# Kernel optimization log

Measured on AMD Instinct MI355X. Metric: run time of the kernel, lower is better.

Reference implementation:

```python
import jax, jax.numpy as jnp
import numpy as np
import math

N_HEADS = 12
HEAD_SIZE = 64
D_MODEL = 768
N_BASIS = 256
LENGTH = 1024
BATCH = 8
INV_SQRT_2PI = 1.0 / math.sqrt(2.0 * math.pi)


def _phi(t):
    # standard normal pdf
    return INV_SQRT_2PI * jnp.exp(-0.5 * t * t)


def _make_basis():
    # get_gaussian_basis_functions: meshgrid(linspace(0,1,N/2), sigmas).flatten()
    sigmas = np.array([0.01, 0.05], dtype=np.float32)
    mus = np.linspace(0.0, 1.0, N_BASIS // 2, dtype=np.float32)
    mu_b = np.repeat(mus, 2)          # [N]
    sigma_b = np.tile(sigmas, N_BASIS // 2)  # [N]
    return jnp.asarray(mu_b), jnp.asarray(sigma_b)


def _make_G(mu_b, sigma_b, klen, ridge=1.0):
    # compute_G: positions (i+1)/l, F[j,i] = psi_j(pos_i), G = F^T (F F^T + I)^{-1}
    pos = jnp.arange(1, klen + 1, dtype=jnp.float32) / klen
    F = _phi((pos[None, :] - mu_b[:, None]) / sigma_b[:, None]) / sigma_b[:, None]  # [N, klen]
    A = F @ F.T + ridge * jnp.eye(N_BASIS, dtype=jnp.float32)
    return F.T @ jnp.linalg.inv(A)  # [klen, N]


def setup_inputs() -> dict:
    key = jax.random.key(0)
    ks = jax.random.split(key, 8)
    sc = 1.0 / math.sqrt(D_MODEL)
    x = jax.random.normal(ks[0], (LENGTH, BATCH, D_MODEL), jnp.float32)
    q = jax.random.normal(ks[1], (LENGTH, BATCH, D_MODEL), jnp.float32)
    Wq = jax.random.normal(ks[2], (D_MODEL, D_MODEL), jnp.float32) * sc
    Wk = jax.random.normal(ks[3], (D_MODEL, D_MODEL), jnp.float32) * sc
    Wv = jax.random.normal(ks[4], (D_MODEL, D_MODEL), jnp.float32) * sc
    Wo = jax.random.normal(ks[5], (D_MODEL, D_MODEL), jnp.float32) * sc
    w_mu = jax.random.normal(ks[6], (N_BASIS,), jnp.float32) * (1.0 / math.sqrt(N_BASIS))
    w_sigma = jax.random.normal(ks[7], (N_BASIS,), jnp.float32) * (1.0 / math.sqrt(N_BASIS))
    mu_b, sigma_b = _make_basis()
    G = _make_G(mu_b, sigma_b, LENGTH)
    return {"x": x, "q": q, "Wq": Wq, "Wk": Wk, "Wv": Wv, "Wo": Wo,
            "w_mu": w_mu, "w_sigma": w_sigma, "mu_b": mu_b, "sigma_b": sigma_b, "G": G}


def reference(x, q, Wq, Wk, Wv, Wo, w_mu, w_sigma, mu_b, sigma_b, G):
    klen, B, d = x.shape
    qlen = q.shape[0]
    H, dh = N_HEADS, HEAD_SIZE
    # value_function: compress memory onto basis coefficients, B_mat: [B, N, d]
    Bmat = jnp.einsum('lbd,ln->bnd', x, G)
    keys = (Bmat @ Wk.T).reshape(B, N_BASIS, H, dh).transpose(0, 2, 1, 3)    # [B,H,N,dh]
    values = (Bmat @ Wv.T).reshape(B, N_BASIS, H, dh).transpose(0, 2, 1, 3)  # [B,H,N,dh]
    query = (q.transpose(1, 0, 2) @ Wq.T).reshape(B, qlen, H, dh).transpose(0, 2, 1, 3)
    scores = jnp.einsum('bhqe,bhne->bhqn', query, keys) / math.sqrt(dh)      # [B,H,q,N]
    # attention distribution parameters (theta -> (mu, sigma_sq) exactly)
    mu = jax.nn.sigmoid(scores @ w_mu)          # [B,H,q]
    sigma_sq = jax.nn.softplus(scores @ w_sigma)  # [B,H,q]
    # ContinuousSoftmax forward: E_{N(mu,sigma_sq)}[psi_j]
    #   = N(mu; mu_b_j, sigma_b_j^2 + sigma_sq)   (product-of-Gaussians integral)
    s = jnp.sqrt(sigma_b[None, None, None, :] ** 2 + sigma_sq[..., None])
    r = _phi((mu[..., None] - mu_b[None, None, None, :]) / s) / s            # [B,H,q,N]
    context = jnp.einsum('bhqn,bhnd->bhqd', r, values)                       # [B,H,q,dh]
    context = context.transpose(0, 2, 1, 3).reshape(B, qlen, H * dh)
    return context @ Wo.T  # [B, qlen, d_model]
```

## Files before the change

### kernel.cpp

```cpp
#include <hip/hip_runtime.h>
#include <hip/hip_bf16.h>
#include <math.h>

#define NHEADS 12
#define HEAD   64
#define DM     768
#define NB     256
#define SLEN   1024
#define NBATCH 8

typedef __bf16 bf16x8 __attribute__((ext_vector_type(8)));
typedef float  f32x4  __attribute__((ext_vector_type(4)));

__device__ __forceinline__ float gload(const void* p, long i, int bf) {
  return bf ? __bfloat162float(((const __hip_bfloat16*)p)[i])
            : ((const float*)p)[i];
}

__global__ void detect_dtype(const void* x, int* flag) {
  __shared__ float red[256];
  int t = threadIdx.x;
  const __hip_bfloat16* p = (const __hip_bfloat16*)x;
  float a = fabsf(__bfloat162float(p[t * 2]));
  float b = fabsf(__bfloat162float(p[t * 2 + 1]));
  float m = fmaxf(a, b);
  red[t] = m;
  __syncthreads();
  for (int s = 128; s > 0; s >>= 1) {
    if (t < s) red[t] = fmaxf(red[t], red[t + s]);
    __syncthreads();
  }
  if (t == 0) flag[0] = (red[0] < 1e4f) ? 1 : 0;
}

__global__ __launch_bounds__(256) void prep(
    const void* __restrict__ Wq, const void* __restrict__ Wk,
    const void* __restrict__ wmu, const void* __restrict__ wsig,
    const void* __restrict__ mub, const void* __restrict__ sigb,
    const void* __restrict__ G, const void* __restrict__ x,
    const void* __restrict__ Wv, const void* __restrict__ Wo,
    float* __restrict__ Wqf, float* __restrict__ Wkf,
    float* __restrict__ wmuf, float* __restrict__ wsigf,
    float* __restrict__ mubf, float* __restrict__ sigbf,
    __hip_bfloat16* __restrict__ Gth, __hip_bfloat16* __restrict__ Gtl,
    __hip_bfloat16* __restrict__ XCh, __hip_bfloat16* __restrict__ XCl,
    __hip_bfloat16* __restrict__ Wvh, __hip_bfloat16* __restrict__ Wvl,
    __hip_bfloat16* __restrict__ Woh, __hip_bfloat16* __restrict__ Wol,
    const int* __restrict__ flagp) {
  __shared__ float tl[64][65];
  const int blk = blockIdx.x, tid = threadIdx.x;
  const int bf = flagp[0];

  if (blk < 1152) {
    const void* src = (blk < 576) ? Wq : Wk;
    float* dst = (blk < 576) ? Wqf : Wkf;
    int rb = (blk < 576) ? blk : blk - 576;
    int i0 = (rb * 256 + tid) * 4;
#pragma unroll
    for (int j = 0; j < 4; j++) dst[i0 + j] = gload(src, i0 + j, bf);
  } else if (blk < 1156) {
    int which = blk - 1152;
    const void* src = (which == 0) ? wmu : (which == 1) ? wsig
                      : (which == 2) ? mub : sigb;
    float* dst = (which == 0) ? wmuf : (which == 1) ? wsigf
                 : (which == 2) ? mubf : sigbf;
    dst[tid] = gload(src, tid, bf);
  } else if (blk < 2756) {
    const void* src;
    __hip_bfloat16 *dh, *dl;
    int R = 1024, C, bx, by;
    if (blk < 1220) {
      int sub = blk - 1156;
      src = G; dh = Gth; dl = Gtl; C = 256; bx = sub % 4; by = sub / 4;
    } else {
      int sub = blk - 1220;
      src = x; dh = XCh; dl = XCl; C = 6144; bx = sub % 96; by = sub / 96;
    }
    int r0 = by * 64, c0 = bx * 64;
    int cl = tid & 63, rl = tid >> 6;
#pragma unroll
    for (int i = 0; i < 16; i++) {
      int rr = rl + i * 4;
      tl[rr][cl] = gload(src, (long)(r0 + rr) * C + c0 + cl, bf);
    }
    __syncthreads();
#pragma unroll
    for (int i = 0; i < 16; i++) {
      int cc = rl + i * 4;
      float f = tl[cl][cc];
      __hip_bfloat16 h = __float2bfloat16(f);
      long o = (long)(c0 + cc) * R + r0 + cl;
      dh[o] = h;
      dl[o] = __float2bfloat16(f - __bfloat162float(h));
    }
  } else {
    const void* src = (blk < 3332) ? Wv : Wo;
    __hip_bfloat16* dh = (blk < 3332) ? Wvh : Woh;
    __hip_bfloat16* dl = (blk < 3332) ? Wvl : Wol;
    int rb = (blk < 3332) ? blk - 2756 : blk - 3332;
    int i0 = (rb * 256 + tid) * 4;
#pragma unroll
    for (int j = 0; j < 4; j++) {
      float f = gload(src, i0 + j, bf);
      __hip_bfloat16 h = __float2bfloat16(f);
      dh[i0 + j] = h;
      dl[i0 + j] = __float2bfloat16(f - __bfloat162float(h));
    }
  }
}

__device__ __forceinline__ void stage512(
    const __hip_bfloat16* __restrict__ src, int ld, __hip_bfloat16* lds, int t) {
  int row = t >> 2;
  int col = ((t & 3) ^ ((t >> 3) & 3)) * 8;
  const __hip_bfloat16* gp = src + (long)row * ld + col;
  __builtin_amdgcn_global_load_lds(
      (const __attribute__((address_space(1))) void*)gp,
      (__attribute__((address_space(3))) void*)((char*)lds + (t >> 6) * 1024),
      16, 0, 0);
}

__device__ __forceinline__ bf16x8 frag_read(
    const __hip_bfloat16* slot, int row, int g) {
  int sl = g ^ ((row >> 1) & 3);
  return *(const bf16x8*)(slot + row * 32 + sl * 8);
}

__global__ __launch_bounds__(512) void mfma_nt_lds(
    const __hip_bfloat16* __restrict__ Ah_g, const __hip_bfloat16* __restrict__ Al_g,
    const __hip_bfloat16* __restrict__ Wh_g, const __hip_bfloat16* __restrict__ Wl_g,
    void* __restrict__ Cout, int K, int lda, int ldb, long a_batch, long c_batch,
    int om, int oh, const int* __restrict__ flagp, int use_flag, int pmask_bf,
    int ksplit, long kslab) {
  int flag = flagp[0];
  int bf = use_flag ? flag : 0;
  __shared__ __hip_bfloat16 S[2][3][4096];

  const int gx = gridDim.x, gy = gridDim.y;
  const int nwg = gx * gy * gridDim.z;
  const int lin = (blockIdx.z * gy + blockIdx.y) * gx + blockIdx.x;
  const int swz = (lin & 7) * (nwg >> 3) + (lin >> 3);
  const int bx = swz % gx;
  const int rem = swz / gx;
  const int by = rem % gy;
  const int bzf = rem / gy;
  const int bz = bzf / ksplit;
  const int kc = bzf - bz * ksplit;
  const int Ks = K / ksplit;
  const int kbeg = kc * Ks, kend = kbeg + Ks;

  const int m0 = by * 128, n0 = bx * 128;
  const int t = threadIdx.x;
  const int lane = t & 63;
  const int r = lane & 15, g = lane >> 4;
  const int wave = t >> 6;
  const int wm = (wave >> 2) * 64, wn = (wave & 3) * 32;

  const __hip_bfloat16* AhR = Ah_g + (long)bz * a_batch + (long)m0 * lda;
  const __hip_bfloat16* AlR = Al_g + (long)bz * a_batch + (long)m0 * lda;
  const __hip_bfloat16* WhR = Wh_g + (long)n0 * ldb;
  const __hip_bfloat16* WlR = Wl_g + (long)n0 * ldb;

  f32x4 zero4 = {0.f, 0.f, 0.f, 0.f};
  f32x4 acc[4][2];
#pragma unroll
  for (int fi = 0; fi < 4; fi++)
#pragma unroll
    for (int fj = 0; fj < 2; fj++) acc[fi][fj] = zero4;

  int nrounds;
  const __hip_bfloat16 *rA[2], *rW[2], *rX[2];
  int rmode[2], rxld[2];
  if (flag) {
    nrounds = 1;
    rA[0] = AhR; rW[0] = WhR; rX[0] = AlR;
    rmode[0] = (pmask_bf & 4) ? 1 : 0; rxld[0] = lda;
  } else {
    nrounds = 2;
    rA[0] = AhR; rW[0] = WhR; rX[0] = WlR; rmode[0] = 2; rxld[0] = ldb;
    rA[1] = AlR; rW[1] = WhR; rX[1] = WhR; rmode[1] = 0; rxld[1] = ldb;
  }

  for (int rd = 0; rd < nrounds; rd++) {
    const __hip_bfloat16* A0 = rA[rd];
    const __hip_bfloat16* W0 = rW[rd];
    const __hip_bfloat16* X0 = rX[rd];
    const int md = rmode[rd], xld = rxld[rd];
    stage512(A0 + kbeg, lda, S[0][0], t);
    stage512(W0 + kbeg, ldb, S[0][1], t);
    if (md) stage512(X0 + kbeg, xld, S[0][2], t);
    __syncthreads();
    int cur = 0;
    for (int k0 = kbeg; k0 < kend; k0 += 32) {
      bf16x8 af[4], bw[2], xf[4];
#pragma unroll
      for (int fi = 0; fi < 4; fi++)
        af[fi] = frag_read(S[cur][0], wm + fi * 16 + r, g);
#pragma unroll
      for (int fj = 0; fj < 2; fj++)
        bw[fj] = frag_read(S[cur][1], wn + fj * 16 + r, g);
      if (md == 1) {
#pragma unroll
        for (int fi = 0; fi < 4; fi++)
          xf[fi] = frag_read(S[cur][2], wm + fi * 16 + r, g);
      } else if (md == 2) {
#pragma unroll
        for (int fj = 0; fj < 2; fj++)
          xf[fj] = frag_read(S[cur][2], wn + fj * 16 + r, g);
      }
      if (k0 + 32 < kend) {
        stage512(A0 + k0 + 32, lda, S[cur ^ 1][0], t);
        stage512(W0 + k0 + 32, ldb, S[cur ^ 1][1], t);
        if (md) stage512(X0 + k0 + 32, xld, S[cur ^ 1][2], t);
      }
#pragma unroll
      for (int fi = 0; fi < 4; fi++)
#pragma unroll
        for (int fj = 0; fj < 2; fj++)
          acc[fi][fj] = __builtin_amdgcn_mfma_f32_16x16x32_bf16(
              af[fi], bw[fj], acc[fi][fj], 0, 0, 0);
      if (md == 1) {
#pragma unroll
        for (int fi = 0; fi < 4; fi++)
#pragma unroll
          for (int fj = 0; fj < 2; fj++)
            acc[fi][fj] = __builtin_amdgcn_mfma_f32_16x16x32_bf16(
                xf[fi], bw[fj], acc[fi][fj], 0, 0, 0);
      } else if (md == 2) {
#pragma unroll
        for (int fi = 0; fi < 4; fi++)
#pragma unroll
          for (int fj = 0; fj < 2; fj++)
            acc[fi][fj] = __builtin_amdgcn_mfma_f32_16x16x32_bf16(
                af[fi], xf[fj], acc[fi][fj], 0, 0, 0);
      }
      __syncthreads();
      cur ^= 1;
    }
  }

  if (ksplit > 1) {
    float* Cf = (float*)Cout + (long)kc * kslab;
#pragma unroll
    for (int fi = 0; fi < 4; fi++)
#pragma unroll
      for (int fj = 0; fj < 2; fj++)
#pragma unroll
        for (int v = 0; v < 4; v++) {
          int m = m0 + wm + fi * 16 + g * 4 + v;
          int n = n0 + wn + fj * 16 + r;
          long off = (long)bz * c_batch + (long)m * om + (long)(n >> 6) * oh + (n & 63);
          Cf[off] = acc[fi][fj][v];
        }
  } else {
#pragma unroll
    for (int fi = 0; fi < 4; fi++)
#pragma unroll
      for (int fj = 0; fj < 2; fj++)
#pragma unroll
        for (int v = 0; v < 4; v++) {
          int m = m0 + wm + fi * 16 + g * 4 + v;
          int n = n0 + wn + fj * 16 + r;
          long off = (long)bz * c_batch + (long)m * om + (long)(n >> 6) * oh + (n & 63);
          float val = acc[fi][fj][v];
          if (bf) ((__hip_bfloat16*)Cout)[off] = __float2bfloat16(val);
          else    ((float*)Cout)[off] = val;
        }
  }
}

__global__ __launch_bounds__(256) void reduce_split(
    const float* __restrict__ slabs, float* __restrict__ outf,
    __hip_bfloat16* __restrict__ dh, __hip_bfloat16* __restrict__ dl) {
  long i0 = ((long)blockIdx.x * 256 + threadIdx.x) * 4;
  f32x4 s = *(const f32x4*)(slabs + i0);
#pragma unroll
  for (int k = 1; k < 4; k++) {
    f32x4 v = *(const f32x4*)(slabs + (long)k * 1572864 + i0);
    s.x += v.x; s.y += v.y; s.z += v.z; s.w += v.w;
  }
  *(f32x4*)(outf + i0) = s;
#pragma unroll
  for (int j = 0; j < 4; j++) {
    float f = s[j];
    __hip_bfloat16 h = __float2bfloat16(f);
    dh[i0 + j] = h;
    dl[i0 + j] = __float2bfloat16(f - __bfloat162float(h));
  }
}

__global__ __launch_bounds__(256) void vtsplit_sum(
    const float* __restrict__ slabs, __hip_bfloat16* __restrict__ dh,
    __hip_bfloat16* __restrict__ dl) {
  __shared__ float tle[64][65];
  const int z = blockIdx.y;
  const int r0 = blockIdx.x * 64;
  int cl = threadIdx.x & 63, rl4 = threadIdx.x >> 6;
#pragma unroll
  for (int i = 0; i < 16; i++) {
    int rr = rl4 + i * 4;
    long idx = (long)z * 16384 + (r0 + rr) * 64 + cl;
    float s = slabs[idx];
#pragma unroll
    for (int k = 1; k < 4; k++) s += slabs[(long)k * 1572864 + idx];
    tle[rr][cl] = s;
  }
  __syncthreads();
#pragma unroll
  for (int i = 0; i < 16; i++) {
    int cc = rl4 + i * 4;
    float f = tle[cl][cc];
    __hip_bfloat16 h = __float2bfloat16(f);
    long o = (long)z * 16384 + (long)cc * 256 + r0 + cl;
    dh[o] = h;
    dl[o] = __float2bfloat16(f - __bfloat162float(h));
  }
}

__global__ __launch_bounds__(256) void bvec(
    const float* __restrict__ Bmat, const float* __restrict__ wmuf,
    const float* __restrict__ wsigf, float* __restrict__ bmu,
    float* __restrict__ bsig) {
  int t = blockIdx.x * 256 + threadIdx.x;
  int w = t / 6144, r = t % 6144;
  const float* wv = w ? wsigf : wmuf;
  float acc = 0.f;
  for (int n = 0; n < NB; n++) acc += wv[n] * Bmat[(long)n * 6144 + r];
  (w ? bsig : bmu)[r] = acc;
}

__global__ __launch_bounds__(256) void kvec(
    const float* __restrict__ Wkf, const float* __restrict__ bmu,
    const float* __restrict__ bsig, float* __restrict__ kmu,
    float* __restrict__ ksig) {
  int t = blockIdx.x * 256 + threadIdx.x;
  int w = t / 6144, r = t % 6144;
  int b = r / 768, c = r % 768;
  const float* bv = (w ? bsig : bmu) + b * 768;
  const float* wk = Wkf + (long)c * 768;
  float acc = 0.f;
  for (int d = 0; d < 768; d++) acc += bv[d] * wk[d];
  (w ? ksig : kmu)[r] = acc;
}

__global__ __launch_bounds__(256) void wqvec(
    const float* __restrict__ Wqf, const float* __restrict__ kmu,
    const float* __restrict__ ksig, float* __restrict__ wqm,
    float* __restrict__ wqs) {
  int t = blockIdx.x * 256 + threadIdx.x;
  int w = t / 73728, r = t % 73728;
  int b = r / 9216, h = (r % 9216) / 768, d = r % 768;
  const float* kv = (w ? ksig : kmu) + b * 768 + h * 64;
  float acc = 0.f;
  for (int dh = 0; dh < 64; dh++)
    acc += Wqf[(long)(h * 64 + dh) * 768 + d] * kv[dh];
  (w ? wqs : wqm)[r] = acc;
}

__global__ __launch_bounds__(256) void amu_kernel(
    const void* __restrict__ q, const float* __restrict__ wqm,
    const float* __restrict__ wqs, float* __restrict__ amu,
    const int* __restrict__ flagp) {
  int bf = flagp[0];
  int lane = threadIdx.x & 63;
  int wave = threadIdx.x >> 6;
  int qrow = blockIdx.x * 4 + wave;
  int b = blockIdx.y;
  float qv[12];
  long base = ((long)qrow * 8 + b) * 768 + lane;
#pragma unroll
  for (int j = 0; j < 12; j++) qv[j] = gload(q, base + 64 * j, bf);
  for (int hh = 0; hh < 24; hh++) {
    const float* vec = (hh < 12) ? (wqm + ((long)b * 12 + hh) * 768)
                                 : (wqs + ((long)b * 12 + hh - 12) * 768);
    float p = 0.f;
#pragma unroll
    for (int j = 0; j < 12; j++) p += qv[j] * vec[lane + 64 * j];
#pragma unroll
    for (int m = 32; m >= 1; m >>= 1) p += __shfl_xor(p, m);
    if (lane == 0) amu[((long)b * 24 + hh) * 1024 + qrow] = p;
  }
}

__global__ __launch_bounds__(256) void attn_mfma(
    const __hip_bfloat16* __restrict__ Vth, const __hip_bfloat16* __restrict__ Vtl,
    const float* __restrict__ amu, const float* __restrict__ mubf,
    const float* __restrict__ sigbf, __hip_bfloat16* __restrict__ Ch,
    __hip_bfloat16* __restrict__ Cl) {
  const int qch = blockIdx.x, h = blockIdx.y, b = blockIdx.z;
  const int t = threadIdx.x;
  const int lane = t & 63, wave = t >> 6;
  const int r = lane & 15, g = lane >> 4;
  const int wq = wave * 32;
  __shared__ float s_mub[NB], s_sb2[NB];
  {
    float sb = sigbf[t];
    s_mub[t] = mubf[t];
    s_sb2[t] = sb * sb;
  }
  __syncthreads();

  float mu_[2], sig_[2];
#pragma unroll
  for (int fi = 0; fi < 2; fi++) {
    int q = qch * 128 + wq + fi * 16 + r;
    float araw = amu[((long)b * 24 + h) * 1024 + q] * 0.125f;
    float sraw = amu[((long)b * 24 + 12 + h) * 1024 + q] * 0.125f;
    mu_[fi] = 1.f / (1.f + expf(-araw));
    sig_[fi] = fmaxf(sraw, 0.f) + log1pf(expf(-fabsf(sraw)));
  }

  const __hip_bfloat16* vhb = Vth + ((long)b * 12 + h) * 16384;
  const __hip_bfloat16* vlb = Vtl + ((long)b * 12 + h) * 16384;

  f32x4 zero4 = {0.f, 0.f, 0.f, 0.f};
  f32x4 acc[2][4];
#pragma unroll
  for (int fi = 0; fi < 2; fi++)
#pragma unroll
    for (int fj = 0; fj < 4; fj++) acc[fi][fj] = zero4;

  for (int ks = 0; ks < 8; ks++) {
    bf16x8 rh[2], rl[2];
#pragma unroll
    for (int fi = 0; fi < 2; fi++) {
      float mu = mu_[fi], sg = sig_[fi];
#pragma unroll
      for (int j = 0; j < 8; j++) {
        int n = ks * 32 + g * 8 + j;
        float inv_s = rsqrtf(s_sb2[n] + sg);
        float tt = (mu - s_mub[n]) * inv_s;
        float rv = 0.3989422804014327f * inv_s *
                   exp2f(-0.7213475204444817f * tt * tt);
        __bf16 hi = (__bf16)rv;
        rh[fi][j] = hi;
        rl[fi][j] = (__bf16)(rv - (float)hi);
      }
    }
#pragma unroll
    for (int fj = 0; fj < 4; fj++) {
      long vo = (long)(fj * 16 + r) * 256 + ks * 32 + g * 8;
      bf16x8 vh = *(const bf16x8*)(vhb + vo);
      bf16x8 vl = *(const bf16x8*)(vlb + vo);
#pragma unroll
      for (int fi = 0; fi < 2; fi++) {
        acc[fi][fj] = __builtin_amdgcn_mfma_f32_16x16x32_bf16(
            rh[fi], vh, acc[fi][fj], 0, 0, 0);
        acc[fi][fj] = __builtin_amdgcn_mfma_f32_16x16x32_bf16(
            rl[fi], vh, acc[fi][fj], 0, 0, 0);
        acc[fi][fj] = __builtin_amdgcn_mfma_f32_16x16x32_bf16(
            rh[fi], vl, acc[fi][fj], 0, 0, 0);
      }
    }
  }

#pragma unroll
  for (int fi = 0; fi < 2; fi++)
#pragma unroll
    for (int fj = 0; fj < 4; fj++)
#pragma unroll
      for (int v = 0; v < 4; v++) {
        int q = qch * 128 + wq + fi * 16 + g * 4 + v;
        int d = fj * 16 + r;
        long off = ((long)(b * SLEN + q)) * DM + h * HEAD + d;
        float f = acc[fi][fj][v];
        __hip_bfloat16 hh = __float2bfloat16(f);
        Ch[off] = hh;
        Cl[off] = __float2bfloat16(f - __bfloat162float(hh));
      }
}

extern "C" void kernel_launch(void* const* d_in, const int* in_sizes, int n_in,
                              void* d_out, int out_size, void* d_ws, size_t ws_size,
                              hipStream_t stream) {
  const void* x    = d_in[0];
  const void* q    = d_in[1];
  const void* Wq   = d_in[2];
  const void* Wk   = d_in[3];
  const void* Wv   = d_in[4];
  const void* Wo   = d_in[5];
  const void* wmu  = d_in[6];
  const void* wsig = d_in[7];
  const void* mub  = d_in[8];
  const void* sigb = d_in[9];
  const void* G    = d_in[10];

  int* flagp = (int*)d_ws;
  float* base = (float*)d_ws + 16;
  float* Wqf   = base;
  float* Wkf   = Wqf + 589824;
  float* wmuf  = Wkf + 589824;
  float* wsigf = wmuf + 256;
  float* mubf  = wsigf + 256;
  float* sigbf = mubf + 256;
  float* Bmat  = sigbf + 256;
  float* slab1 = Bmat + 1572864;
  float* wqm   = slab1 + 6291456;
  float* wqs   = wqm + 73728;
  float* amu   = wqs + 73728;
  float* bmu   = amu + 196608;
  float* bsig  = bmu + 6144;
  float* kmu   = bsig + 6144;
  float* ksig  = kmu + 6144;
  __hip_bfloat16* Wvh = (__hip_bfloat16*)(ksig + 6144);
  __hip_bfloat16* Wvl = Wvh + 589824;
  __hip_bfloat16* Woh = Wvl + 589824;
  __hip_bfloat16* Wol = Woh + 589824;
  __hip_bfloat16* Gth = Wol + 589824;
  __hip_bfloat16* Gtl = Gth + 262144;
  __hip_bfloat16* Bh  = Gtl + 262144;
  __hip_bfloat16* Bl  = Bh + 1572864;
  __hip_bfloat16* XCh = Bl + 1572864;
  __hip_bfloat16* XCl = XCh + 6291456;
  float* slab2 = (float*)XCh;
  __hip_bfloat16* Vth = XCl + 6291456;
  __hip_bfloat16* Vtl = Vth + 1572864;

  detect_dtype<<<1, 256, 0, stream>>>(x, flagp);

  prep<<<3908, 256, 0, stream>>>(
      Wq, Wk, wmu, wsig, mub, sigb, G, x, Wv, Wo,
      Wqf, Wkf, wmuf, wsigf, mubf, sigbf,
      Gth, Gtl, XCh, XCl, Wvh, Wvl, Woh, Wol, flagp);

  mfma_nt_lds<<<dim3(48, 2, 4), 512, 0, stream>>>(
      Gth, Gtl, XCh, XCl, slab1, 1024, 1024, 1024,
      0, 0, 6144, 64, flagp, 0,
      1, 4, 1572864);

  reduce_split<<<1536, 256, 0, stream>>>(slab1, Bmat, Bh, Bl);

  mfma_nt_lds<<<dim3(6, 2, 32), 512, 0, stream>>>(
      Bh, Bl, Wvh, Wvl, slab2, 768, 6144, 768,
      768, 196608, 64, 16384, flagp, 0,
      5, 4, 1572864);

  vtsplit_sum<<<dim3(4, 96), 256, 0, stream>>>(slab2, Vth, Vtl);

  bvec<<<48, 256, 0, stream>>>(Bmat, wmuf, wsigf, bmu, bsig);
  kvec<<<48, 256, 0, stream>>>(Wkf, bmu, bsig, kmu, ksig);
  wqvec<<<576, 256, 0, stream>>>(Wqf, kmu, ksig, wqm, wqs);
  amu_kernel<<<dim3(256, 8), 256, 0, stream>>>(q, wqm, wqs, amu, flagp);

  attn_mfma<<<dim3(8, 12, 8), 256, 0, stream>>>(
      Vth, Vtl, amu, mubf, sigbf, XCh, XCl);

  mfma_nt_lds<<<dim3(6, 64, 1), 512, 0, stream>>>(
      XCh, XCl, Woh, Wol, d_out, 768, 768, 768,
      0, 0, 768, 64, flagp, 1,
      5, 1, 0);
}
```

Measured before the change: 363.7 us.

## Use 256-thread GEMM blocks with 64x64 warp tiles and prefetch-two pipeline

The GEMM kernel moves from 512 threads with 64x32 per-wave tiles to 256 threads with 64x64 per-wave tiles. Each thread now issues two global-to-LDS loads per stage, and the loop prefetches two k-steps ahead using explicit vmcnt waits and raw barriers in place of __syncthreads. The aim is better MFMA-to-LDS-read reuse per wave and more overlap between global loads and compute. In exchange it raises register pressure from the larger accumulator set and relies on hand-counted waitcnt values, which must match the number of outstanding loads.

```diff
diff --git a/kernel.cpp b/kernel.cpp
--- a/kernel.cpp
+++ b/kernel.cpp
@@ -109,15 +109,19 @@
   }
 }
 
-__device__ __forceinline__ void stage512(
+__device__ __forceinline__ void stage256(
     const __hip_bfloat16* __restrict__ src, int ld, __hip_bfloat16* lds, int t) {
   int row = t >> 2;
   int col = ((t & 3) ^ ((t >> 3) & 3)) * 8;
-  const __hip_bfloat16* gp = src + (long)row * ld + col;
-  __builtin_amdgcn_global_load_lds(
-      (const __attribute__((address_space(1))) void*)gp,
-      (__attribute__((address_space(3))) void*)((char*)lds + (t >> 6) * 1024),
-      16, 0, 0);
+  int wavebase = (t >> 6) * 1024;
+#pragma unroll
+  for (int i = 0; i < 2; i++) {
+    const __hip_bfloat16* gp = src + (long)(i * 64 + row) * ld + col;
+    __builtin_amdgcn_global_load_lds(
+        (const __attribute__((address_space(1))) void*)gp,
+        (__attribute__((address_space(3))) void*)((char*)lds + i * 4096 + wavebase),
+        16, 0, 0);
+  }
 }
 
 __device__ __forceinline__ bf16x8 frag_read(
@@ -126,7 +130,7 @@
   return *(const bf16x8*)(slot + row * 32 + sl * 8);
 }
 
-__global__ __launch_bounds__(512) void mfma_nt_lds(
+__global__ __launch_bounds__(256) void mfma_nt_lds(
     const __hip_bfloat16* __restrict__ Ah_g, const __hip_bfloat16* __restrict__ Al_g,
     const __hip_bfloat16* __restrict__ Wh_g, const __hip_bfloat16* __restrict__ Wl_g,
     void* __restrict__ Cout, int K, int lda, int ldb, long a_batch, long c_batch,
@@ -147,14 +151,15 @@
   const int bz = bzf / ksplit;
   const int kc = bzf - bz * ksplit;
   const int Ks = K / ksplit;
-  const int kbeg = kc * Ks, kend = kbeg + Ks;
+  const int kbeg = kc * Ks;
+  const int nk = Ks >> 5;
 
   const int m0 = by * 128, n0 = bx * 128;
   const int t = threadIdx.x;
   const int lane = t & 63;
   const int r = lane & 15, g = lane >> 4;
   const int wave = t >> 6;
-  const int wm = (wave >> 2) * 64, wn = (wave & 3) * 32;
+  const int wm = (wave >> 1) * 64, wn = (wave & 1) * 64;
 
   const __hip_bfloat16* AhR = Ah_g + (long)bz * a_batch + (long)m0 * lda;
   const __hip_bfloat16* AlR = Al_g + (long)bz * a_batch + (long)m0 * lda;
@@ -162,11 +167,11 @@
   const __hip_bfloat16* WlR = Wl_g + (long)n0 * ldb;
 
   f32x4 zero4 = {0.f, 0.f, 0.f, 0.f};
-  f32x4 acc[4][2];
+  f32x4 acc[4][4];
 #pragma unroll
   for (int fi = 0; fi < 4; fi++)
 #pragma unroll
-    for (int fj = 0; fj < 2; fj++) acc[fi][fj] = zero4;
+    for (int fj = 0; fj < 4; fj++) acc[fi][fj] = zero4;
 
   int nrounds;
   const __hip_bfloat16 *rA[2], *rW[2], *rX[2];
@@ -186,56 +191,75 @@
     const __hip_bfloat16* W0 = rW[rd];
     const __hip_bfloat16* X0 = rX[rd];
     const int md = rmode[rd], xld = rxld[rd];
-    stage512(A0 + kbeg, lda, S[0][0], t);
-    stage512(W0 + kbeg, ldb, S[0][1], t);
-    if (md) stage512(X0 + kbeg, xld, S[0][2], t);
-    __syncthreads();
-    int cur = 0;
-    for (int k0 = kbeg; k0 < kend; k0 += 32) {
-      bf16x8 af[4], bw[2], xf[4];
+    stage256(A0 + kbeg, lda, S[0][0], t);
+    stage256(W0 + kbeg, ldb, S[0][1], t);
+    if (md) stage256(X0 + kbeg, xld, S[0][2], t);
+    stage256(A0 + kbeg + 32, lda, S[1][0], t);
+    stage256(W0 + kbeg + 32, ldb, S[1][1], t);
+    if (md) stage256(X0 + kbeg + 32, xld, S[1][2], t);
+
+    for (int i = 0; i < nk; i++) {
+      if (i < nk - 1) {
+        if (md) asm volatile("s_waitcnt vmcnt(6)" ::: "memory");
+        else    asm volatile("s_waitcnt vmcnt(4)" ::: "memory");
+      } else {
+        asm volatile("s_waitcnt vmcnt(0)" ::: "memory");
+      }
+      __builtin_amdgcn_s_barrier();
+      asm volatile("" ::: "memory");
+
+      const __hip_bfloat16* SA = S[i & 1][0];
+      const __hip_bfloat16* SW = S[i & 1][1];
+      const __hip_bfloat16* SX = S[i & 1][2];
+      bf16x8 af[4], bw[4], xf[4];
 #pragma unroll
       for (int fi = 0; fi < 4; fi++)
-        af[fi] = frag_read(S[cur][0], wm + fi * 16 + r, g);
-#pragma unroll
-      for (int fj = 0; fj < 2; fj++)
-        bw[fj] = frag_read(S[cur][1], wn + fj * 16 + r, g);
+        af[fi] = frag_read(SA, wm + fi * 16 + r, g);
+#pragma unroll
+      for (int fj = 0; fj < 4; fj++)
+        bw[fj] = frag_read(SW, wn + fj * 16 + r, g);
       if (md == 1) {
 #pragma unroll
         for (int fi = 0; fi < 4; fi++)
-          xf[fi] = frag_read(S[cur][2], wm + fi * 16 + r, g);
+          xf[fi] = frag_read(SX, wm + fi * 16 + r, g);
       } else if (md == 2) {
 #pragma unroll
-        for (int fj = 0; fj < 2; fj++)
-          xf[fj] = frag_read(S[cur][2], wn + fj * 16 + r, g);
-      }
-      if (k0 + 32 < kend) {
-        stage512(A0 + k0 + 32, lda, S[cur ^ 1][0], t);
-        stage512(W0 + k0 + 32, ldb, S[cur ^ 1][1], t);
-        if (md) stage512(X0 + k0 + 32, xld, S[cur ^ 1][2], t);
-      }
+        for (int fj = 0; fj < 4; fj++)
+          xf[fj] = frag_read(SX, wn + fj * 16 + r, g);
+      }
+      asm volatile("s_waitcnt lgkmcnt(0)" ::: "memory");
+      __builtin_amdgcn_sched_barrier(0);
+      __builtin_amdgcn_s_barrier();
+      asm volatile("" ::: "memory");
+
+      if (i + 2 < nk) {
+        const long ko = kbeg + (long)(i + 2) * 32;
+        stage256(A0 + ko, lda, S[i & 1][0], t);
+        stage256(W0 + ko, ldb, S[i & 1][1], t);
+        if (md) stage256(X0 + ko, xld, S[i & 1][2], t);
+      }
+
 #pragma unroll
       for (int fi = 0; fi < 4; fi++)
 #pragma unroll
-        for (int fj = 0; fj < 2; fj++)
+        for (int fj = 0; fj < 4; fj++)
           acc[fi][fj] = __builtin_amdgcn_mfma_f32_16x16x32_bf16(
               af[fi], bw[fj], acc[fi][fj], 0, 0, 0);
       if (md == 1) {
 #pragma unroll
         for (int fi = 0; fi < 4; fi++)
 #pragma unroll
-          for (int fj = 0; fj < 2; fj++)
+          for (int fj = 0; fj < 4; fj++)
             acc[fi][fj] = __builtin_amdgcn_mfma_f32_16x16x32_bf16(
                 xf[fi], bw[fj], acc[fi][fj], 0, 0, 0);
       } else if (md == 2) {
 #pragma unroll
         for (int fi = 0; fi < 4; fi++)
 #pragma unroll
-          for (int fj = 0; fj < 2; fj++)
+          for (int fj = 0; fj < 4; fj++)
             acc[fi][fj] = __builtin_amdgcn_mfma_f32_16x16x32_bf16(
                 af[fi], xf[fj], acc[fi][fj], 0, 0, 0);
       }
-      __syncthreads();
-      cur ^= 1;
     }
   }
 
@@ -244,7 +268,7 @@
 #pragma unroll
     for (int fi = 0; fi < 4; fi++)
 #pragma unroll
-      for (int fj = 0; fj < 2; fj++)
+      for (int fj = 0; fj < 4; fj++)
 #pragma unroll
         for (int v = 0; v < 4; v++) {
           int m = m0 + wm + fi * 16 + g * 4 + v;
@@ -256,7 +280,7 @@
 #pragma unroll
     for (int fi = 0; fi < 4; fi++)
 #pragma unroll
-      for (int fj = 0; fj < 2; fj++)
+      for (int fj = 0; fj < 4; fj++)
 #pragma unroll
         for (int v = 0; v < 4; v++) {
           int m = m0 + wm + fi * 16 + g * 4 + v;
@@ -523,14 +547,14 @@
       Wqf, Wkf, wmuf, wsigf, mubf, sigbf,
       Gth, Gtl, XCh, XCl, Wvh, Wvl, Woh, Wol, flagp);
 
-  mfma_nt_lds<<<dim3(48, 2, 4), 512, 0, stream>>>(
+  mfma_nt_lds<<<dim3(48, 2, 4), 256, 0, stream>>>(
       Gth, Gtl, XCh, XCl, slab1, 1024, 1024, 1024,
       0, 0, 6144, 64, flagp, 0,
       1, 4, 1572864);
 
   reduce_split<<<1536, 256, 0, stream>>>(slab1, Bmat, Bh, Bl);
 
-  mfma_nt_lds<<<dim3(6, 2, 32), 512, 0, stream>>>(
+  mfma_nt_lds<<<dim3(6, 2, 32), 256, 0, stream>>>(
       Bh, Bl, Wvh, Wvl, slab2, 768, 6144, 768,
       768, 196608, 64, 16384, flagp, 0,
       5, 4, 1572864);
@@ -545,7 +569,7 @@
   attn_mfma<<<dim3(8, 12, 8), 256, 0, stream>>>(
       Vth, Vtl, amu, mubf, sigbf, XCh, XCl);
 
-  mfma_nt_lds<<<dim3(6, 64, 1), 512, 0, stream>>>(
+  mfma_nt_lds<<<dim3(6, 64, 1), 256, 0, stream>>>(
       XCh, XCl, Woh, Wol, d_out, 768, 768, 768,
       0, 0, 768, 64, flagp, 1,
       5, 1, 0);
```

Measured after the change: 340.1 us. 6.5% less time.
